# Optimization experiments

Measured on AMD Instinct MI355X. Metric: run time of the kernel, lower is better.

Reference implementation:

```python
import jax, jax.numpy as jnp
import numpy as np

HW, WW, NH = 8, 8, 6  # window height/width, num heads


def _rel_pos_index(hw, ww):
    # Swin relative position index, computed statically with numpy
    coords = np.stack(np.meshgrid(np.arange(hw), np.arange(ww), indexing='ij'))  # [2,hw,ww]
    cf = coords.reshape(2, -1)
    rel = (cf[:, :, None] - cf[:, None, :]).transpose(1, 2, 0).astype(np.int64)  # [N,N,2]
    rel[:, :, 0] += hw - 1
    rel[:, :, 1] += ww - 1
    rel[:, :, 0] *= 2 * ww - 1
    return jnp.asarray(rel.sum(-1))  # [N,N]


def setup_inputs() -> dict:
    key = jax.random.key(0)
    ks = jax.random.split(key, 4)
    b, h, w, c = 8, 192, 192, 192
    return {
        'x': jax.random.normal(ks[0], (b, h * w, c), jnp.float32),
        'wqkv_w': jax.random.normal(ks[1], (c, 3 * c), jnp.float32) * 0.02,
        'wqkv_b': jnp.zeros((3 * c,), jnp.float32),
        'wp_w': jax.random.normal(ks[2], (c, c), jnp.float32) * 0.02,
        'wp_b': jnp.zeros((c,), jnp.float32),
        'bias_table': jax.random.normal(ks[3], ((2 * HW - 1) * (2 * WW - 1), NH), jnp.float32) * 0.02,
        'h': 192,
        'w': 192,
    }


def reference(x, wqkv_w, wqkv_b, wp_w, wp_b, bias_table, h, w):
    b, n, c = x.shape
    hd = c // NH
    pad_b = (HW - h % HW) % HW
    pad_r = (WW - w % WW) % WW
    H, W = h + pad_b, w + pad_r
    Hn, Wn = H // HW, W // WW
    N = HW * WW

    xi = x.reshape(b, h, w, c)
    xi = jnp.pad(xi, ((0, 0), (0, pad_b), (0, pad_r), (0, 0)))  # [b,H,W,c]

    qkv = xi @ wqkv_w + wqkv_b  # [b,H,W,3c]
    # partition into windows and split heads: -> [3, nW, NH, N, hd]
    qkv = qkv.reshape(b, Hn, HW, Wn, WW, 3, NH, hd)
    qkv = qkv.transpose(5, 0, 1, 3, 6, 2, 4, 7).reshape(3, b * Hn * Wn, NH, N, hd)
    q, k, v = qkv[0], qkv[1], qkv[2]

    idx = _rel_pos_index(HW, WW)  # [N,N]
    bias = bias_table[idx].transpose(2, 0, 1)  # [NH,N,N]

    scores = jnp.einsum('whqd,whkd->whqk', q, k) / np.sqrt(hd).astype(np.float32)
    scores = scores + bias[None]
    attn = jax.nn.softmax(scores, axis=-1)
    y = jnp.einsum('whqk,whkd->whqd', attn, v)  # [nW,NH,N,hd]

    # merge windows back to image: [b,H,W,c]
    y = y.reshape(b, Hn, Wn, NH, HW, WW, hd)
    y = y.transpose(0, 1, 4, 2, 5, 3, 6).reshape(b, H, W, c)
    out = y @ wp_w + wp_b
    out = out[:, :h, :w, :].reshape(b, h * w, c)
    return out
```

## Files before the change

### kernel.cpp

```cpp
#include <hip/hip_runtime.h>
#include <hip/hip_bf16.h>

typedef unsigned short u16;
typedef __attribute__((ext_vector_type(8))) short bf16x8;
typedef __attribute__((ext_vector_type(4))) float f32x4;

#define MFMA16(a, b, c) __builtin_amdgcn_mfma_f32_16x16x32_bf16(a, b, c, 0, 0, 0)

__device__ __forceinline__ u16 f2bf(float f) {
  union { float f; unsigned u; } v; v.f = f;
  unsigned r = v.u + 0x7fffu + ((v.u >> 16) & 1u);
  return (u16)(r >> 16);
}

__device__ __forceinline__ unsigned pkbf(float lo, float hi) {
  union { __hip_bfloat162 h; unsigned u; } v;
  v.h = __hip_bfloat162(__float2bfloat16(lo), __float2bfloat16(hi));
  return v.u;
}

__device__ __forceinline__ bf16x8 xform(f32x4 a0, f32x4 a1, int srcA, bool hi) {
  unsigned p0 = pkbf(a0[0], a0[1]), p1 = pkbf(a0[2], a0[3]);
  unsigned p2 = pkbf(a1[0], a1[1]), p3 = pkbf(a1[2], a1[3]);
  int srcB = srcA + 16;
  unsigned u0 = __shfl((int)p0, srcA), u1 = __shfl((int)p1, srcA);
  unsigned u2 = __shfl((int)p2, srcA), u3 = __shfl((int)p3, srcA);
  unsigned v0 = __shfl((int)p0, srcB), v1 = __shfl((int)p1, srcB);
  unsigned v2 = __shfl((int)p2, srcB), v3 = __shfl((int)p3, srcB);
  union { bf16x8 v; unsigned w[4]; } o;
  o.w[0] = hi ? u2 : u0; o.w[1] = hi ? u3 : u1;
  o.w[2] = hi ? v2 : v0; o.w[3] = hi ? v3 : v1;
  return o.v;
}

__global__ void pack_kernel(const float* __restrict__ wqkv_w,
                            const float* __restrict__ wp_w,
                            const float* __restrict__ bias_table,
                            u16* __restrict__ wpack, u16* __restrict__ wppack,
                            float* __restrict__ biasf) {
  int i = blockIdx.x * 256 + threadIdx.x;
  if (i < 110592) {
    int j = i & 7, l = (i >> 3) & 63;
    int rest = i >> 9;
    int ks = rest % 6, nt = rest / 6;
    int k = ks * 32 + (l >> 4) * 8 + j;
    int n = nt * 16 + (l & 15);
    wpack[i] = f2bf(wqkv_w[k * 576 + n]);
  } else if (i < 147456) {
    int i2 = i - 110592;
    int j = i2 & 7, l = (i2 >> 3) & 63;
    int rest = i2 >> 9;
    int ks = rest % 6, nt = rest / 6;
    int k = ks * 32 + (l >> 4) * 8 + j;
    int n = nt * 16 + (l & 15);
    wppack[i2] = f2bf(wp_w[k * 192 + n]);
  } else if (i < 172032) {
    int i2 = i - 147456;
    int r = i2 & 3, lane = (i2 >> 2) & 63, mt = (i2 >> 8) & 3, nt = (i2 >> 10) & 3, h = i2 >> 12;
    int q = nt * 16 + (lane & 15);
    int kk = mt * 16 + (lane >> 4) * 4 + r;
    int idx = ((q >> 3) - (kk >> 3) + 7) * 15 + ((q & 7) - (kk & 7) + 7);
    biasf[i2] = bias_table[idx * 6 + h];
  }
}

__global__ __launch_bounds__(64, 2) void attn6(
    const float* __restrict__ x, const u16* __restrict__ wpack,
    const float* __restrict__ wqkv_b, const float* __restrict__ biasf,
    u16* __restrict__ y) {
  __shared__ u16 xs[12288];
  const int lane = threadIdx.x & 63;
  const int w = (blockIdx.x & 7) * 576 + (blockIdx.x >> 3);
  const int bb = w / 576, rem = w - bb * 576;
  const int wy = rem / 24, wx = rem - (rem / 24) * 24;
  const size_t xbase = (size_t)bb * 36864;
  const int g = lane >> 4, li = lane & 15;
  const int srcA = (lane & 16) * 2 + li;
  const bool hi = lane >= 32;

  const int pix0 = (wy * 8 + (li >> 3)) * 192 + wx * 8 + (li & 7);
  const float* xr = x + (xbase + pix0) * 192 + g * 8;
  const u16* wbase = wpack + lane * 8;

  const float scale = 0.17677669529663687f;
  const f32x4 zero4 = {0.f, 0.f, 0.f, 0.f};

#pragma unroll
  for (int mt = 0; mt < 4; ++mt)
#pragma unroll
    for (int ks = 0; ks < 6; ++ks) {
      const float* p = xr + mt * 73728 + ks * 32;
      float4 f0 = *(const float4*)p;
      float4 f1 = *(const float4*)(p + 4);
      union { bf16x8 v; unsigned u[4]; } o;
      o.u[0] = pkbf(f0.x, f0.y); o.u[1] = pkbf(f0.z, f0.w);
      o.u[2] = pkbf(f1.x, f1.y); o.u[3] = pkbf(f1.z, f1.w);
      *(bf16x8*)(xs + ((mt * 6 + ks) * 64 + lane) * 8) = o.v;
    }
  __syncthreads();

#pragma unroll 1
  for (int h = 0; h < 6; ++h) {
    f32x4 qt[2][4], kt[2][4];
#pragma unroll
    for (int i = 0; i < 2; ++i)
#pragma unroll
      for (int mt = 0; mt < 4; ++mt) { qt[i][mt] = zero4; kt[i][mt] = zero4; }
#pragma unroll
    for (int ks = 0; ks < 6; ++ks) {
      bf16x8 af[4];
#pragma unroll
      for (int mt = 0; mt < 4; ++mt)
        af[mt] = *(const bf16x8*)(xs + ((mt * 6 + ks) * 64 + lane) * 8);
#pragma unroll
      for (int i = 0; i < 2; ++i) {
        bf16x8 wq = *(const bf16x8*)(wbase + ((2 * h + i) * 6 + ks) * 512);
        bf16x8 wk = *(const bf16x8*)(wbase + ((12 + 2 * h + i) * 6 + ks) * 512);
#pragma unroll
        for (int mt = 0; mt < 4; ++mt) {
          qt[i][mt] = MFMA16(wq, af[mt], qt[i][mt]);
          kt[i][mt] = MFMA16(wk, af[mt], kt[i][mt]);
        }
      }
    }

    f32x4 bq0 = *(const f32x4*)(wqkv_b + h * 32 + g * 4);
    f32x4 bq1 = *(const f32x4*)(wqkv_b + h * 32 + 16 + g * 4);
    f32x4 bk0 = *(const f32x4*)(wqkv_b + 192 + h * 32 + g * 4);
    f32x4 bk1 = *(const f32x4*)(wqkv_b + 192 + h * 32 + 16 + g * 4);
    bf16x8 qf[4], kf[4];
#pragma unroll
    for (int mt = 0; mt < 4; ++mt) {
      qf[mt] = xform((qt[0][mt] + bq0) * scale, (qt[1][mt] + bq1) * scale, srcA, hi);
      kf[mt] = xform(kt[0][mt] + bk0, kt[1][mt] + bk1, srcA, hi);
    }

    f32x4 va[4][2];
#pragma unroll
    for (int mt = 0; mt < 4; ++mt) { va[mt][0] = zero4; va[mt][1] = zero4; }
#pragma unroll
    for (int ks = 0; ks < 6; ++ks) {
      bf16x8 af[4];
#pragma unroll
      for (int mt = 0; mt < 4; ++mt)
        af[mt] = *(const bf16x8*)(xs + ((mt * 6 + ks) * 64 + lane) * 8);
      bf16x8 wv0 = *(const bf16x8*)(wbase + ((24 + 2 * h) * 6 + ks) * 512);
      bf16x8 wv1 = *(const bf16x8*)(wbase + ((25 + 2 * h) * 6 + ks) * 512);
#pragma unroll
      for (int mt = 0; mt < 4; ++mt) {
        va[mt][0] = MFMA16(af[mt], wv0, va[mt][0]);
        va[mt][1] = MFMA16(af[mt], wv1, va[mt][1]);
      }
    }
    float bva0 = wqkv_b[384 + h * 32 + li], bva1 = wqkv_b[384 + h * 32 + 16 + li];
    bf16x8 vf[2][2];
#pragma unroll
    for (int i = 0; i < 2; ++i) {
      float bv = i ? bva1 : bva0;
#pragma unroll
      for (int ks2 = 0; ks2 < 2; ++ks2)
        vf[i][ks2] = xform(va[ks2 * 2][i] + bv, va[ks2 * 2 + 1][i] + bv, srcA, hi);
    }

    const float* bfh = biasf + h * 4096 + lane * 4;
    f32x4 yt[2][4];
#pragma unroll
    for (int nt = 0; nt < 4; ++nt) { yt[0][nt] = zero4; yt[1][nt] = zero4; }
#pragma unroll
    for (int nt = 0; nt < 4; ++nt) {
      f32x4 em[4];
#pragma unroll
      for (int mt = 0; mt < 4; ++mt) {
        f32x4 stn = MFMA16(kf[mt], qf[nt], zero4);
        em[mt] = stn + *(const f32x4*)(bfh + (nt * 4 + mt) * 256);
      }
      float mx = -1e30f;
#pragma unroll
      for (int mt = 0; mt < 4; ++mt)
        mx = fmaxf(mx, fmaxf(fmaxf(em[mt][0], em[mt][1]), fmaxf(em[mt][2], em[mt][3])));
      mx = fmaxf(mx, __shfl_xor(mx, 16));
      mx = fmaxf(mx, __shfl_xor(mx, 32));
      float s = 0.f;
#pragma unroll
      for (int mt = 0; mt < 4; ++mt)
#pragma unroll
        for (int r = 0; r < 4; ++r) { em[mt][r] = __expf(em[mt][r] - mx); s += em[mt][r]; }
      s += __shfl_xor(s, 16);
      s += __shfl_xor(s, 32);
      float inv = 1.0f / s;
#pragma unroll
      for (int ks2 = 0; ks2 < 2; ++ks2) {
        bf16x8 pf = xform(em[ks2 * 2] * inv, em[ks2 * 2 + 1] * inv, srcA, hi);
        yt[0][nt] = MFMA16(vf[0][ks2], pf, yt[0][nt]);
        yt[1][nt] = MFMA16(vf[1][ks2], pf, yt[1][nt]);
      }
    }

    u16* yp = y + (xbase + pix0) * 192 + h * 32 + g * 8;
#pragma unroll
    for (int mt = 0; mt < 4; ++mt) {
      bf16x8 yfr = xform(yt[0][mt], yt[1][mt], srcA, hi);
      *(bf16x8*)(yp + mt * 73728) = yfr;
    }
  }
}

__global__ __launch_bounds__(256, 2) void proj_kernel(
    const u16* __restrict__ y, const u16* __restrict__ wppack,
    const float* __restrict__ wp_b, float* __restrict__ out) {
  const int tid = threadIdx.x;
  const int lane = tid & 63, wv = tid >> 6;
  const int g = lane >> 4, li = lane & 15;
  const size_t row0 = (size_t)blockIdx.x * 128 + wv * 32;
  const f32x4 zero4 = {0.f, 0.f, 0.f, 0.f};
  f32x4 acc[2][12];
#pragma unroll
  for (int mt = 0; mt < 2; ++mt)
#pragma unroll
    for (int nt = 0; nt < 12; ++nt) acc[mt][nt] = zero4;
#pragma unroll
  for (int ks = 0; ks < 6; ++ks) {
    bf16x8 af[2];
#pragma unroll
    for (int mt = 0; mt < 2; ++mt)
      af[mt] = *(const bf16x8*)(y + (row0 + mt * 16 + li) * 192 + ks * 32 + g * 8);
#pragma unroll
    for (int nt = 0; nt < 12; ++nt) {
      bf16x8 bf = *(const bf16x8*)(wppack + (nt * 6 + ks) * 512 + lane * 8);
      acc[0][nt] = MFMA16(af[0], bf, acc[0][nt]);
      acc[1][nt] = MFMA16(af[1], bf, acc[1][nt]);
    }
  }
#pragma unroll
  for (int nt = 0; nt < 12; ++nt) {
    float bb = wp_b[nt * 16 + li];
#pragma unroll
    for (int mt = 0; mt < 2; ++mt)
#pragma unroll
      for (int r = 0; r < 4; ++r)
        out[(row0 + mt * 16 + g * 4 + r) * 192 + nt * 16 + li] = acc[mt][nt][r] + bb;
  }
}

extern "C" void kernel_launch(void* const* d_in, const int* in_sizes, int n_in,
                              void* d_out, int out_size, void* d_ws, size_t ws_size,
                              hipStream_t stream) {
  (void)in_sizes; (void)n_in; (void)out_size; (void)ws_size;
  const float* x          = (const float*)d_in[0];
  const float* wqkv_w     = (const float*)d_in[1];
  const float* wqkv_b     = (const float*)d_in[2];
  const float* wp_w       = (const float*)d_in[3];
  const float* wp_b       = (const float*)d_in[4];
  const float* bias_table = (const float*)d_in[5];
  float* out = (float*)d_out;
  char* ws = (char*)d_ws;
  u16* wpack   = (u16*)(ws);
  u16* wppack  = (u16*)(ws + 221184);
  float* biasf = (float*)(ws + 294912);
  u16* y       = (u16*)(ws + 393216);

  pack_kernel<<<672, 256, 0, stream>>>(wqkv_w, wp_w, bias_table, wpack, wppack, biasf);
  attn6<<<4608, 64, 0, stream>>>(x, wpack, wqkv_b, biasf, y);
  proj_kernel<<<2304, 256, 0, stream>>>(y, wppack, wp_b, out);
}
```

Before: 327.8 us.

## Split attention heads across two waves per window and store y head-major

Each attention block now runs two wavefronts: both cooperatively convert the window's x tile into shared memory, and each wave then handles three of the six heads. This raises parallelism per window and shortens the per-wave serial head loop. Q and K projections are computed in separate phases to cut live accumulator registers, and launch bounds change to 128 threads with 3 blocks per CU. The intermediate y is stored in a head-major layout ([head][pixel][32]) and the projection kernel reads it that way, which changes the access pattern of both the writes and the reads.

```diff
diff --git a/kernel.cpp b/kernel.cpp
--- a/kernel.cpp
+++ b/kernel.cpp
@@ -64,12 +64,13 @@
   }
 }
 
-__global__ __launch_bounds__(64, 2) void attn6(
+__global__ __launch_bounds__(128, 3) void attn6(
     const float* __restrict__ x, const u16* __restrict__ wpack,
     const float* __restrict__ wqkv_b, const float* __restrict__ biasf,
     u16* __restrict__ y) {
   __shared__ u16 xs[12288];
   const int lane = threadIdx.x & 63;
+  const int wv = threadIdx.x >> 6;
   const int w = (blockIdx.x & 7) * 576 + (blockIdx.x >> 3);
   const int bb = w / 576, rem = w - bb * 576;
   const int wy = rem / 24, wx = rem - (rem / 24) * 24;
@@ -86,7 +87,8 @@
   const f32x4 zero4 = {0.f, 0.f, 0.f, 0.f};
 
 #pragma unroll
-  for (int mt = 0; mt < 4; ++mt)
+  for (int mi = 0; mi < 2; ++mi) {
+    const int mt = wv * 2 + mi;
 #pragma unroll
     for (int ks = 0; ks < 6; ++ks) {
       const float* p = xr + mt * 73728 + ks * 32;
@@ -97,15 +99,16 @@
       o.u[2] = pkbf(f1.x, f1.y); o.u[3] = pkbf(f1.z, f1.w);
       *(bf16x8*)(xs + ((mt * 6 + ks) * 64 + lane) * 8) = o.v;
     }
+  }
   __syncthreads();
 
 #pragma unroll 1
-  for (int h = 0; h < 6; ++h) {
-    f32x4 qt[2][4], kt[2][4];
+  for (int h = wv * 3; h < wv * 3 + 3; ++h) {
+    f32x4 qt[2][4];
 #pragma unroll
     for (int i = 0; i < 2; ++i)
 #pragma unroll
-      for (int mt = 0; mt < 4; ++mt) { qt[i][mt] = zero4; kt[i][mt] = zero4; }
+      for (int mt = 0; mt < 4; ++mt) qt[i][mt] = zero4;
 #pragma unroll
     for (int ks = 0; ks < 6; ++ks) {
       bf16x8 af[4];
@@ -115,25 +118,41 @@
 #pragma unroll
       for (int i = 0; i < 2; ++i) {
         bf16x8 wq = *(const bf16x8*)(wbase + ((2 * h + i) * 6 + ks) * 512);
-        bf16x8 wk = *(const bf16x8*)(wbase + ((12 + 2 * h + i) * 6 + ks) * 512);
-#pragma unroll
-        for (int mt = 0; mt < 4; ++mt) {
-          qt[i][mt] = MFMA16(wq, af[mt], qt[i][mt]);
-          kt[i][mt] = MFMA16(wk, af[mt], kt[i][mt]);
-        }
-      }
-    }
-
+#pragma unroll
+        for (int mt = 0; mt < 4; ++mt) qt[i][mt] = MFMA16(wq, af[mt], qt[i][mt]);
+      }
+    }
     f32x4 bq0 = *(const f32x4*)(wqkv_b + h * 32 + g * 4);
     f32x4 bq1 = *(const f32x4*)(wqkv_b + h * 32 + 16 + g * 4);
+    bf16x8 qf[4];
+#pragma unroll
+    for (int mt = 0; mt < 4; ++mt)
+      qf[mt] = xform((qt[0][mt] + bq0) * scale, (qt[1][mt] + bq1) * scale, srcA, hi);
+
+    f32x4 kt[2][4];
+#pragma unroll
+    for (int i = 0; i < 2; ++i)
+#pragma unroll
+      for (int mt = 0; mt < 4; ++mt) kt[i][mt] = zero4;
+#pragma unroll
+    for (int ks = 0; ks < 6; ++ks) {
+      bf16x8 af[4];
+#pragma unroll
+      for (int mt = 0; mt < 4; ++mt)
+        af[mt] = *(const bf16x8*)(xs + ((mt * 6 + ks) * 64 + lane) * 8);
+#pragma unroll
+      for (int i = 0; i < 2; ++i) {
+        bf16x8 wk = *(const bf16x8*)(wbase + ((12 + 2 * h + i) * 6 + ks) * 512);
+#pragma unroll
+        for (int mt = 0; mt < 4; ++mt) kt[i][mt] = MFMA16(wk, af[mt], kt[i][mt]);
+      }
+    }
     f32x4 bk0 = *(const f32x4*)(wqkv_b + 192 + h * 32 + g * 4);
     f32x4 bk1 = *(const f32x4*)(wqkv_b + 192 + h * 32 + 16 + g * 4);
-    bf16x8 qf[4], kf[4];
-#pragma unroll
-    for (int mt = 0; mt < 4; ++mt) {
-      qf[mt] = xform((qt[0][mt] + bq0) * scale, (qt[1][mt] + bq1) * scale, srcA, hi);
+    bf16x8 kf[4];
+#pragma unroll
+    for (int mt = 0; mt < 4; ++mt)
       kf[mt] = xform(kt[0][mt] + bk0, kt[1][mt] + bk1, srcA, hi);
-    }
 
     f32x4 va[4][2];
 #pragma unroll
@@ -196,11 +215,11 @@
       }
     }
 
-    u16* yp = y + (xbase + pix0) * 192 + h * 32 + g * 8;
+    u16* yp = y + (size_t)h * 9437184 + (xbase + pix0) * 32 + g * 8;
 #pragma unroll
     for (int mt = 0; mt < 4; ++mt) {
       bf16x8 yfr = xform(yt[0][mt], yt[1][mt], srcA, hi);
-      *(bf16x8*)(yp + mt * 73728) = yfr;
+      *(bf16x8*)(yp + mt * 12288) = yfr;
     }
   }
 }
@@ -223,7 +242,7 @@
     bf16x8 af[2];
 #pragma unroll
     for (int mt = 0; mt < 2; ++mt)
-      af[mt] = *(const bf16x8*)(y + (row0 + mt * 16 + li) * 192 + ks * 32 + g * 8);
+      af[mt] = *(const bf16x8*)(y + (size_t)ks * 9437184 + (row0 + mt * 16 + li) * 32 + g * 8);
 #pragma unroll
     for (int nt = 0; nt < 12; ++nt) {
       bf16x8 bf = *(const bf16x8*)(wppack + (nt * 6 + ks) * 512 + lane * 8);
@@ -260,6 +279,6 @@
   u16* y       = (u16*)(ws + 393216);
 
   pack_kernel<<<672, 256, 0, stream>>>(wqkv_w, wp_w, bias_table, wpack, wppack, biasf);
-  attn6<<<4608, 64, 0, stream>>>(x, wpack, wqkv_b, biasf, y);
+  attn6<<<4608, 128, 0, stream>>>(x, wpack, wqkv_b, biasf, y);
   proj_kernel<<<2304, 256, 0, stream>>>(y, wppack, wp_b, out);
 }
```

Result: slower. 432.9 us (+32.1%).
